# Performance work log

Hardware: AMD Instinct MI355X
Metric: run time of the kernel (lower is better)

## Reference

```python
import jax, jax.numpy as jnp
import numpy as np


def setup_inputs() -> dict:
    key = jax.random.key(0)
    k1, k2 = jax.random.split(key)
    mesh_3D = jax.random.uniform(k1, (100, 100, 100, 3), dtype=jnp.float32)
    receiver_pos = jax.random.uniform(k2, (128, 3), dtype=jnp.float32)
    return {"mesh_3D": mesh_3D, "receiver_pos": receiver_pos}


def reference(mesh_3D, receiver_pos):
    # Flatten mesh to [L, 3]
    pts = mesh_3D.reshape(-1, 3)
    L = pts.shape[0]
    B = receiver_pos.shape[0]
    # Squared distances [B, L]; argmin of sqrt(d2) == argmin of d2 (sqrt is monotone),
    # so skipping the sqrt gives the same indices as the torch code.
    d2 = jnp.sum((receiver_pos[:, None, :] - pts[None, :, :]) ** 2, axis=-1)
    min_index = jnp.argmin(d2, axis=1).astype(jnp.int32)  # [B]
    # One-hot over the mesh. The original loop scatters with the *whole* min_index
    # tensor (zero-initialized) at every iteration, so for B > 1 index 0 also ends
    # up set to 1. We reproduce that behavior faithfully.
    one_hot = jnp.zeros((L, 1), dtype=pts.dtype).at[min_index, 0].set(1.0)
    if B > 1:
        one_hot = one_hot.at[0, 0].set(1.0)
    closest_points = pts[min_index]  # [B, 3]
    input_tensor = jnp.concatenate([pts, one_hot], axis=1).astype(jnp.float32)  # [L, 4]
    return input_tensor, closest_points, min_index
```

## Files before the change

### kernel.cpp

```cpp
#include <hip/hip_runtime.h>


#define NRECV 128
#define TILE 512
#define BLK 512
#define NWAVE (BLK / 64)
#define CELL_STRIDE 16

typedef unsigned long long u64;

__global__ __launch_bounds__(128) void k_init(u64* __restrict__ cells, int n) {
  int i = blockIdx.x * 128 + threadIdx.x;
  if (i < n) cells[i] = ~0ull;
}

__global__ __launch_bounds__(BLK) void k_main(
    const float* __restrict__ pts, const float* __restrict__ recv,
    u64* __restrict__ cells, int nbanks, float* __restrict__ out,
    int L, int ntiles) {
  __shared__ float4 sp4[TILE + 1];
  __shared__ u64 sm[NWAVE][NRECV];

  const int tid = threadIdx.x;
  const int g = tid >> 6;
  const int c = tid & 31;
  const int ph = (tid >> 5) & 1;

  float rx[4], ry[4], rz[4];
#pragma unroll
  for (int k = 0; k < 4; ++k) {
    rx[k] = recv[(c + 32 * k) * 3 + 0];
    ry[k] = recv[(c + 32 * k) * 3 + 1];
    rz[k] = recv[(c + 32 * k) * 3 + 2];
  }

  float bd[4] = {1e30f, 1e30f, 1e30f, 1e30f};
  int bi[4] = {0, 0, 0, 0};

  for (int t = blockIdx.x; t < ntiles; t += gridDim.x) {
    const int base = t * TILE;
    const int cnt = min(TILE, L - base);

    if (tid < cnt) {
      const int gi = base + tid;
      float4 v;
      v.x = pts[3 * gi + 0];
      v.y = pts[3 * gi + 1];
      v.z = pts[3 * gi + 2];
      v.w = 0.0f;
      sp4[tid] = v;
      reinterpret_cast<float4*>(out)[gi] = v;
    }
    if (tid == 0 && cnt < TILE)
      sp4[cnt] = make_float4(1e30f, 1e30f, 1e30f, 0.0f);
    __syncthreads();

#pragma unroll 2
    for (int p2 = 2 * g; p2 < cnt; p2 += 2 * NWAVE) {
      const int p = p2 + ph;
      const float4 q = sp4[p];
#pragma unroll
      for (int k = 0; k < 4; ++k) {
        const float dx = q.x - rx[k];
        const float dy = q.y - ry[k];
        const float dz = q.z - rz[k];
        const float d = fmaf(dz, dz, fmaf(dy, dy, dx * dx));
        const bool cc = d < bd[k];
        bd[k] = cc ? d : bd[k];
        bi[k] = cc ? (base + p) : bi[k];
      }
    }
    __syncthreads();
  }

  u64 key[4];
#pragma unroll
  for (int k = 0; k < 4; ++k) {
    key[k] = ((u64)__float_as_uint(bd[k]) << 32) | (unsigned int)bi[k];
    const u64 o = __shfl_xor(key[k], 32, 64);
    key[k] = o < key[k] ? o : key[k];
  }
  if (ph == 0) {
#pragma unroll
    for (int k = 0; k < 4; ++k) sm[g][c + 32 * k] = key[k];
  }
  __syncthreads();
  if (tid < NRECV) {
    u64 best = sm[0][tid];
#pragma unroll
    for (int w = 1; w < NWAVE; ++w) {
      const u64 o = sm[w][tid];
      best = o < best ? o : best;
    }
    const int bank = blockIdx.x & (nbanks - 1);
    atomicMin(&cells[(size_t)(bank * NRECV + tid) * CELL_STRIDE], best);
  }
}

__global__ __launch_bounds__(128) void k_finalize(
    const u64* __restrict__ cells, int nbanks,
    const float* __restrict__ pts, float* __restrict__ out, int L) {
  const int r = threadIdx.x;
  u64 best = ~0ull;
  for (int b = 0; b < nbanks; ++b) {
    const u64 o = cells[(size_t)(b * NRECV + r) * CELL_STRIDE];
    best = o < best ? o : best;
  }
  const unsigned int idx = (unsigned int)(best & 0xffffffffu);
  const size_t Lo = (size_t)L * 4;
  out[Lo + (size_t)r * 3 + 0] = pts[(size_t)idx * 3 + 0];
  out[Lo + (size_t)r * 3 + 1] = pts[(size_t)idx * 3 + 1];
  out[Lo + (size_t)r * 3 + 2] = pts[(size_t)idx * 3 + 2];
  out[Lo + (size_t)NRECV * 3 + r] = (float)idx;
  out[(size_t)idx * 4 + 3] = 1.0f;
  if (r == 0) out[3] = 1.0f;
}

extern "C" void kernel_launch(void* const* d_in, const int* in_sizes, int n_in,
                              void* d_out, int out_size, void* d_ws, size_t ws_size,
                              hipStream_t stream) {
  const float* pts = (const float*)d_in[0];
  const float* recv = (const float*)d_in[1];
  float* out = (float*)d_out;
  u64* cells = (u64*)d_ws;

  const int L = in_sizes[0] / 3;
  const int ntiles = (L + TILE - 1) / TILE;

  const int nbanks =
      (ws_size >= (size_t)4 * NRECV * CELL_STRIDE * sizeof(u64)) ? 4 : 1;
  const int ncell_u64 = nbanks * NRECV * CELL_STRIDE;

  int grid = 512;
  if (grid > ntiles) grid = ntiles;

  k_init<<<(ncell_u64 + 127) / 128, 128, 0, stream>>>(cells, ncell_u64);
  k_main<<<grid, BLK, 0, stream>>>(pts, recv, cells, nbanks, out, L, ntiles);
  k_finalize<<<1, 128, 0, stream>>>(cells, nbanks, pts, out, L);
}
```

Before: 98.35 us.

## Replace atomic-min banks with per-block staging and parallel finalize reduction

Each block now writes its per-receiver best key to a staging buffer instead of doing atomicMin into banked cells, so the init kernel goes away. Finalize becomes 128 blocks of 64 threads that each reduce one receiver across all blocks with wave shuffles. The grid grows to up to 1024 blocks, the copy of points to the output uses nontemporal stores, and the inner loop unroll rises to 4. This removes one launch and the atomic contention, at the cost of a larger workspace and more staging traffic.

```diff
diff --git a/kernel.cpp b/kernel.cpp
--- a/kernel.cpp
+++ b/kernel.cpp
@@ -5,20 +5,15 @@
 #define TILE 512
 #define BLK 512
 #define NWAVE (BLK / 64)
-#define CELL_STRIDE 16
+#define GRID_MAX 1024
 
 typedef unsigned long long u64;
-
-__global__ __launch_bounds__(128) void k_init(u64* __restrict__ cells, int n) {
-  int i = blockIdx.x * 128 + threadIdx.x;
-  if (i < n) cells[i] = ~0ull;
-}
+typedef float f4 __attribute__((ext_vector_type(4)));
 
 __global__ __launch_bounds__(BLK) void k_main(
     const float* __restrict__ pts, const float* __restrict__ recv,
-    u64* __restrict__ cells, int nbanks, float* __restrict__ out,
-    int L, int ntiles) {
-  __shared__ float4 sp4[TILE + 1];
+    u64* __restrict__ stage, float* __restrict__ out, int L, int ntiles) {
+  __shared__ f4 sp4[TILE + 1];
   __shared__ u64 sm[NWAVE][NRECV];
 
   const int tid = threadIdx.x;
@@ -43,22 +38,25 @@
 
     if (tid < cnt) {
       const int gi = base + tid;
-      float4 v;
+      f4 v;
       v.x = pts[3 * gi + 0];
       v.y = pts[3 * gi + 1];
       v.z = pts[3 * gi + 2];
       v.w = 0.0f;
       sp4[tid] = v;
-      reinterpret_cast<float4*>(out)[gi] = v;
+      __builtin_nontemporal_store(v, reinterpret_cast<f4*>(out) + gi);
     }
-    if (tid == 0 && cnt < TILE)
-      sp4[cnt] = make_float4(1e30f, 1e30f, 1e30f, 0.0f);
+    if (tid == 0 && cnt < TILE) {
+      f4 pad;
+      pad.x = 1e30f; pad.y = 1e30f; pad.z = 1e30f; pad.w = 0.0f;
+      sp4[cnt] = pad;
+    }
     __syncthreads();
 
-#pragma unroll 2
+#pragma unroll 4
     for (int p2 = 2 * g; p2 < cnt; p2 += 2 * NWAVE) {
       const int p = p2 + ph;
-      const float4 q = sp4[p];
+      const f4 q = sp4[p];
 #pragma unroll
       for (int k = 0; k < 4; ++k) {
         const float dx = q.x - rx[k];
@@ -92,28 +90,36 @@
       const u64 o = sm[w][tid];
       best = o < best ? o : best;
     }
-    const int bank = blockIdx.x & (nbanks - 1);
-    atomicMin(&cells[(size_t)(bank * NRECV + tid) * CELL_STRIDE], best);
+    stage[(size_t)blockIdx.x * NRECV + tid] = best;
   }
 }
 
-__global__ __launch_bounds__(128) void k_finalize(
-    const u64* __restrict__ cells, int nbanks,
+__global__ __launch_bounds__(64) void k_finalize(
+    const u64* __restrict__ stage, int nblocks,
     const float* __restrict__ pts, float* __restrict__ out, int L) {
-  const int r = threadIdx.x;
+  const int r = blockIdx.x;
+  const int tid = threadIdx.x;
+
   u64 best = ~0ull;
-  for (int b = 0; b < nbanks; ++b) {
-    const u64 o = cells[(size_t)(b * NRECV + r) * CELL_STRIDE];
+  for (int j = tid; j < nblocks; j += 64) {
+    const u64 k = stage[(size_t)j * NRECV + r];
+    best = k < best ? k : best;
+  }
+#pragma unroll
+  for (int off = 32; off > 0; off >>= 1) {
+    const u64 o = __shfl_down(best, off);
     best = o < best ? o : best;
   }
-  const unsigned int idx = (unsigned int)(best & 0xffffffffu);
-  const size_t Lo = (size_t)L * 4;
-  out[Lo + (size_t)r * 3 + 0] = pts[(size_t)idx * 3 + 0];
-  out[Lo + (size_t)r * 3 + 1] = pts[(size_t)idx * 3 + 1];
-  out[Lo + (size_t)r * 3 + 2] = pts[(size_t)idx * 3 + 2];
-  out[Lo + (size_t)NRECV * 3 + r] = (float)idx;
-  out[(size_t)idx * 4 + 3] = 1.0f;
-  if (r == 0) out[3] = 1.0f;
+  if (tid == 0) {
+    const unsigned int idx = (unsigned int)(best & 0xffffffffu);
+    const size_t Lo = (size_t)L * 4;
+    out[Lo + (size_t)r * 3 + 0] = pts[(size_t)idx * 3 + 0];
+    out[Lo + (size_t)r * 3 + 1] = pts[(size_t)idx * 3 + 1];
+    out[Lo + (size_t)r * 3 + 2] = pts[(size_t)idx * 3 + 2];
+    out[Lo + (size_t)NRECV * 3 + r] = (float)idx;
+    out[(size_t)idx * 4 + 3] = 1.0f;
+    if (r == 0) out[3] = 1.0f;
+  }
 }
 
 extern "C" void kernel_launch(void* const* d_in, const int* in_sizes, int n_in,
@@ -122,19 +128,19 @@
   const float* pts = (const float*)d_in[0];
   const float* recv = (const float*)d_in[1];
   float* out = (float*)d_out;
-  u64* cells = (u64*)d_ws;
+  u64* stage = (u64*)d_ws;
 
   const int L = in_sizes[0] / 3;
   const int ntiles = (L + TILE - 1) / TILE;
 
-  const int nbanks =
-      (ws_size >= (size_t)4 * NRECV * CELL_STRIDE * sizeof(u64)) ? 4 : 1;
-  const int ncell_u64 = nbanks * NRECV * CELL_STRIDE;
+  int grid = GRID_MAX;
+  if (grid > ntiles) grid = ntiles;
+  const size_t need = (size_t)grid * NRECV * sizeof(u64);
+  if (need > ws_size) {
+    grid = (int)(ws_size / (NRECV * sizeof(u64)));
+    if (grid < 1) grid = 1;
+  }
 
-  int grid = 512;
-  if (grid > ntiles) grid = ntiles;
-
-  k_init<<<(ncell_u64 + 127) / 128, 128, 0, stream>>>(cells, ncell_u64);
-  k_main<<<grid, BLK, 0, stream>>>(pts, recv, cells, nbanks, out, L, ntiles);
-  k_finalize<<<1, 128, 0, stream>>>(cells, nbanks, pts, out, L);
+  k_main<<<grid, BLK, 0, stream>>>(pts, recv, stage, out, L, ntiles);
+  k_finalize<<<NRECV, 64, 0, stream>>>(stage, grid, pts, out, L);
 }
```

Result: no change. 98.23 us (-0.1%).
